# Kernel tuning notes

Hardware: AMD Instinct MI355X
Metric: run time of the kernel (lower is better)

## Reference

```python
import jax, jax.numpy as jnp
import numpy as np

V, D, DI, S, B, NI = 32000, 1024, 768, 512, 8, 197
EPS = 1e-5

def _ln(x, g, b):
    m = jnp.mean(x, axis=-1, keepdims=True)
    v = jnp.var(x, axis=-1, keepdims=True)
    return (x - m) * jax.lax.rsqrt(v + EPS) * g + b

def _pos_enc(seq_len, d):
    pos = np.arange(seq_len)[:, None].astype(np.float32)
    i = np.arange(0, d, 2).astype(np.float32)
    ang = pos / np.power(10000.0, i / d)
    pe = np.zeros((seq_len, d), dtype=np.float32)
    pe[:, 0::2] = np.sin(ang)
    pe[:, 1::2] = np.cos(ang)
    return jnp.asarray(pe)

def setup_inputs() -> dict:
    key = jax.random.key(0)
    ks = jax.random.split(key, 24)
    def rn(k, shape, scale=0.02):
        return jax.random.normal(k, shape, dtype=jnp.float32) * scale
    return {
        'tokens': jax.random.randint(ks[0], (B, S), 0, V),
        'img_emb': jax.random.normal(ks[1], (B, NI, DI), dtype=jnp.float32),
        'emb_table': rn(ks[2], (V, D), 1.0),
        'Wq1': rn(ks[3], (D, D)), 'bq1': jnp.zeros((D,), jnp.float32),
        'Wk1': rn(ks[4], (D, D)), 'bk1': jnp.zeros((D,), jnp.float32),
        'Wv1': rn(ks[5], (D, D)), 'bv1': jnp.zeros((D,), jnp.float32),
        'g1': jnp.ones((D,), jnp.float32), 'b1': jnp.zeros((D,), jnp.float32),
        'Wq2': rn(ks[6], (D, D)), 'bq2': jnp.zeros((D,), jnp.float32),
        'Wk2': rn(ks[7], (DI, D)), 'bk2': jnp.zeros((D,), jnp.float32),
        'Wv2': rn(ks[8], (DI, D)), 'bv2': jnp.zeros((D,), jnp.float32),
        'g2': jnp.ones((D,), jnp.float32), 'b2': jnp.zeros((D,), jnp.float32),
        'Wp': rn(ks[9], (D, V)), 'bp': jnp.zeros((V,), jnp.float32),
    }

def _forward(tokens, img_emb, emb_table, Wq1, bq1, Wk1, bk1, Wv1, bv1, g1, b1,
             Wq2, bq2, Wk2, bk2, Wv2, bv2, g2, b2, Wp, bp):
    scale = 1.0 / jnp.sqrt(jnp.float32(D))
    x = emb_table[tokens] + _pos_enc(S, D)[None]  # [B,S,D]
    # masked (causal) self-attention
    Q = x @ Wq1 + bq1
    K = x @ Wk1 + bk1
    Vv = x @ Wv1 + bv1
    attn = jnp.einsum('bqd,bkd->bqk', Q, K) * scale
    causal = jnp.tril(jnp.ones((S, S), dtype=bool))
    attn = jnp.where(causal[None], attn, -jnp.inf)
    A = jax.nn.softmax(attn, axis=-1)
    x = _ln(A @ Vv + x, g1, b1)
    # cross-attention over image tokens
    Q2 = x @ Wq2 + bq2
    K2 = img_emb @ Wk2 + bk2
    V2 = img_emb @ Wv2 + bv2
    A2 = jax.nn.softmax(jnp.einsum('bqd,bkd->bqk', Q2, K2) * scale, axis=-1)
    x = _ln(A2 @ V2 + x, g2, b2)
    # vocab projection (note: Decoder.forward never calls self.ff)
    return x @ Wp + bp  # [B,S,V]

def reference(tokens, img_emb, emb_table, Wq1, bq1, Wk1, bk1, Wv1, bv1, g1, b1,
              Wq2, bq2, Wk2, bk2, Wv2, bv2, g2, b2, Wp, bp):
    return _forward(tokens, img_emb, emb_table, Wq1, bq1, Wk1, bk1, Wv1, bv1, g1, b1,
                    Wq2, bq2, Wk2, bk2, Wv2, bv2, g2, b2, Wp, bp)
```

## Files before the change

### kernel.cpp

```cpp
#include <hip/hip_runtime.h>
#include <hip/hip_bf16.h>


#define DEV __device__ __forceinline__

typedef __bf16 bf16x8 __attribute__((ext_vector_type(8)));
typedef float f32x4 __attribute__((ext_vector_type(4)));
typedef float f32x16 __attribute__((ext_vector_type(16)));
typedef unsigned int u32;
typedef __hip_bfloat16 bf16;

DEV void llds16(const void* g, void* l) {
  __builtin_amdgcn_global_load_lds((const __attribute__((address_space(1))) u32*)g,
                                   (__attribute__((address_space(3))) u32*)l, 16, 0, 0);
}

DEV float wredsum(float v){
#pragma unroll
  for (int o = 32; o; o >>= 1) v += __shfl_xor(v, o, 64);
  return v;
}
DEV float wredmax(float v){
#pragma unroll
  for (int o = 32; o; o >>= 1) v = fmaxf(v, __shfl_xor(v, o, 64));
  return v;
}

DEV void store_out(float* p, float v){ *p = v; }
DEV void store_out(bf16* p, float v){ *p = __float2bfloat16(v); }

__global__ __launch_bounds__(512, 1) void gemm256_kernel(
    const bf16* __restrict__ A, const bf16* __restrict__ Bt, float* __restrict__ C,
    const float* __restrict__ bias, int M, int N, int K, int lda, int ldb, int ldc)
{
  __shared__ alignas(16) char lds[131072];
  const int tid  = threadIdx.x;
  const int wave = tid >> 6, lane = tid & 63;
  const int l31 = lane & 31, lh = lane >> 5;
  const int wr = wave >> 2, wc = wave & 3;
  const int koff = (((lane & 3) ^ ((lane >> 3) & 3)) << 3);

  const int nbx = M >> 8;
  const int nwg = nbx * (N >> 8);
  int id = blockIdx.x;
  int g = (nwg & 7) ? id : ((id & 7) * (nwg >> 3) + (id >> 3));
  const int row0 = (g % nbx) * 256, col0 = (g / nbx) * 256;
  const int NT = K >> 5;
  const int srow = lane >> 2;

  auto stageA = [&](int t) {
    char* base = lds + (t & 3) * 32768;
    const int kk = (t << 5) + koff;
#pragma unroll
    for (int j = 0; j < 2; j++) {
      const int seg = j * 8 + wave;
      llds16(A + (long)(row0 + seg * 16 + srow) * lda + kk, base + seg * 1024);
    }
  };
  auto stageB = [&](int t) {
    char* base = lds + (t & 3) * 32768 + 16384;
    const int kk = (t << 5) + koff;
#pragma unroll
    for (int j = 0; j < 2; j++) {
      const int seg = j * 8 + wave;
      llds16(Bt + (long)(col0 + seg * 16 + srow) * ldb + kk, base + seg * 1024);
    }
  };

  f32x16 acc[4][2] = {};

  stageA(0); stageB(0); stageA(1); stageB(1); stageA(2); stageB(2);
  asm volatile("s_waitcnt vmcnt(8)" ::: "memory");
  __builtin_amdgcn_s_barrier();
  __builtin_amdgcn_sched_barrier(0);

  for (int t = 0; t < NT; t++) {
    const char* As = lds + (t & 3) * 32768;
    const char* Bs = As + 16384;
    bf16x8 af[4][2], bfv[2][2];
#pragma unroll
    for (int m = 0; m < 4; m++) {
      const int r = wr * 128 + m * 32 + l31;
      const int key = (r >> 1) & 3;
#pragma unroll
      for (int ks = 0; ks < 2; ks++)
        af[m][ks] = *(const bf16x8*)(As + (r << 6) + (((lh + 2 * ks) ^ key) << 4));
    }
#pragma unroll
    for (int n = 0; n < 2; n++) {
      const int r = wc * 64 + n * 32 + l31;
      const int key = (r >> 1) & 3;
#pragma unroll
      for (int ks = 0; ks < 2; ks++)
        bfv[n][ks] = *(const bf16x8*)(Bs + (r << 6) + (((lh + 2 * ks) ^ key) << 4));
    }
    if (t + 3 < NT) { stageA(t + 3); stageB(t + 3); }
    __builtin_amdgcn_sched_barrier(0);
    __builtin_amdgcn_s_setprio(1);
#pragma unroll
    for (int m = 0; m < 4; m++)
#pragma unroll
      for (int n = 0; n < 2; n++)
#pragma unroll
        for (int ks = 0; ks < 2; ks++)
          acc[m][n] = __builtin_amdgcn_mfma_f32_32x32x16_bf16(af[m][ks], bfv[n][ks], acc[m][n], 0, 0, 0);
    __builtin_amdgcn_s_setprio(0);
    __builtin_amdgcn_sched_barrier(0);
    if (t < NT - 3)       asm volatile("s_waitcnt vmcnt(8)" ::: "memory");
    else if (t == NT - 3) asm volatile("s_waitcnt vmcnt(4)" ::: "memory");
    else                  asm volatile("s_waitcnt vmcnt(0)" ::: "memory");
    __builtin_amdgcn_s_barrier();
    __builtin_amdgcn_sched_barrier(0);
  }

#pragma unroll
  for (int n = 0; n < 2; n++) {
    const int c = col0 + wc * 64 + n * 32 + l31;
    const float bb = bias ? bias[c] : 0.0f;
#pragma unroll
    for (int m = 0; m < 4; m++) {
      const int rb = row0 + wr * 128 + m * 32 + 4 * lh;
#pragma unroll
      for (int r = 0; r < 16; r++) {
        const int row = rb + (r & 3) + 8 * (r >> 2);
        C[(long)row * ldc + c] = acc[m][n][r] + bb;
      }
    }
  }
}

template<typename OutT>
__global__ __launch_bounds__(256) void gemm_bt_kernel(
    const bf16* __restrict__ A, const bf16* __restrict__ Bt, OutT* __restrict__ C,
    const float* __restrict__ bias, int M, int N, int K,
    int lda, int ldb, int ldc, long sA, long sB, long sC)
{
  A  += (long)blockIdx.z * sA;
  Bt += (long)blockIdx.z * sB;
  C  += (long)blockIdx.z * sC;
  __shared__ alignas(16) bf16 As[128*32];
  __shared__ alignas(16) bf16 Bs[128*32];
  const int tid = threadIdx.x;
  const int wave = tid >> 6, lane = tid & 63;
  const int lo = lane & 15, hi = lane >> 4;
  const int hi2 = hi ^ ((lo >> 1) & 3);
  const int wr = wave >> 1, wc = wave & 1;
  const int row0 = blockIdx.x * 128, col0 = blockIdx.y * 128;
  const int srow  = lane >> 2;
  const int skoff = (((lane & 3) ^ ((lane >> 3) & 3)) << 3);

  f32x4 acc[4][4] = {};

  for (int k0 = 0; k0 < K; k0 += 32) {
#pragma unroll
    for (int c = 0; c < 2; ++c) {
      const int seg = c*4 + wave;
      int ra = row0 + seg*16 + srow; ra = ra < M ? ra : M-1;
      llds16(A + (long)ra*lda + (k0 + skoff), (char*)As + seg*1024);
      int rb = col0 + seg*16 + srow; rb = rb < N ? rb : N-1;
      llds16(Bt + (long)rb*ldb + (k0 + skoff), (char*)Bs + seg*1024);
    }
    __syncthreads();
    bf16x8 af[4], bfv[4];
#pragma unroll
    for (int m = 0; m < 4; m++)
      af[m] = *(const bf16x8*)((const char*)As + (wr*64 + m*16 + lo)*64 + hi2*16);
#pragma unroll
    for (int n = 0; n < 4; n++)
      bfv[n] = *(const bf16x8*)((const char*)Bs + (wc*64 + n*16 + lo)*64 + hi2*16);
#pragma unroll
    for (int m = 0; m < 4; m++)
#pragma unroll
      for (int n = 0; n < 4; n++)
        acc[m][n] = __builtin_amdgcn_mfma_f32_16x16x32_bf16(af[m], bfv[n], acc[m][n], 0, 0, 0);
    __syncthreads();
  }

#pragma unroll
  for (int m = 0; m < 4; m++) {
    const int rbase = row0 + wr*64 + m*16 + hi*4;
#pragma unroll
    for (int n = 0; n < 4; n++) {
      const int cc = col0 + wc*64 + n*16 + lo;
      if (cc >= N) continue;
      const float bb = bias ? bias[cc] : 0.0f;
#pragma unroll
      for (int j = 0; j < 4; j++) {
        const int rr = rbase + j;
        if (rr < M) store_out(&C[(long)rr*ldc + cc], acc[m][n][j] + bb);
      }
    }
  }
}

__global__ __launch_bounds__(256) void wprep4_kernel(
    const float* W0, const float* W1, const float* W2, const float* W3,
    bf16* T0, bf16* T1, bf16* T2, bf16* T3, int K, int N)
{
  const int z = blockIdx.z;
  const float* W = z == 0 ? W0 : z == 1 ? W1 : z == 2 ? W2 : W3;
  bf16* T = z == 0 ? T0 : z == 1 ? T1 : z == 2 ? T2 : T3;
  __shared__ bf16 t[32][33];
  const int k0 = blockIdx.x * 32, n0 = blockIdx.y * 32;
  const int tx = threadIdx.x & 31, ty = threadIdx.x >> 5;
#pragma unroll
  for (int i = 0; i < 4; i++)
    t[ty + i*8][tx] = __float2bfloat16(W[(long)(k0 + ty + i*8)*N + n0 + tx]);
  __syncthreads();
#pragma unroll
  for (int i = 0; i < 4; i++)
    T[(long)(n0 + ty + i*8)*K + k0 + tx] = t[tx][ty + i*8];
}

__global__ __launch_bounds__(256) void transpose_pad_kernel(
    const bf16* __restrict__ in, bf16* __restrict__ out,
    int R, int Cc, int inLD, int outLD, long inBatch, long outBatch)
{
  in  += (long)blockIdx.z * inBatch;
  out += (long)blockIdx.z * outBatch;
  __shared__ bf16 t[32][33];
  const int r0 = blockIdx.x * 32, c0 = blockIdx.y * 32;
  const int tx = threadIdx.x & 31, ty = threadIdx.x >> 5;
#pragma unroll
  for (int i = 0; i < 4; i++) {
    const int r = r0 + ty + i*8;
    bf16 v = __float2bfloat16(0.0f);
    if (r < R) v = in[(long)r*inLD + c0 + tx];
    t[ty + i*8][tx] = v;
  }
  __syncthreads();
#pragma unroll
  for (int i = 0; i < 4; i++) {
    const int oc = r0 + tx;
    const int orow = c0 + ty + i*8;
    if (oc < outLD) out[(long)orow*outLD + oc] = t[tx][ty + i*8];
  }
}

__global__ __launch_bounds__(256) void concat_bias_kernel(
    const float* a, const float* b, const float* c, int n1, int n2, int n3, float* out)
{
  const int i = blockIdx.x * 256 + threadIdx.x;
  if (i >= n1 + n2 + n3) return;
  out[i] = i < n1 ? a[i] : (i < n1 + n2 ? b[i - n1] : c[i - n1 - n2]);
}

__global__ __launch_bounds__(256) void embed_kernel(
    const int* __restrict__ tok, const float* __restrict__ tbl,
    float* __restrict__ xf, bf16* __restrict__ xb)
{
  const int row = blockIdx.x;
  const int s = row & 511;
  const float pos = (float)s;
  const float* te = tbl + (long)tok[row] * 1024;
  const int d0 = threadIdx.x * 4;
  float4 v = *(const float4*)(te + d0);
  float o[4] = {v.x, v.y, v.z, v.w};
#pragma unroll
  for (int k = 0; k < 4; k++) {
    const int d = d0 + k;
    const int i2 = d & ~1;
    const float ang = pos * powf(10000.0f, -(float)i2 * (1.0f/1024.0f));
    o[k] += (d & 1) ? cosf(ang) : sinf(ang);
  }
  *(float4*)(xf + (long)row*1024 + d0) = make_float4(o[0], o[1], o[2], o[3]);
#pragma unroll
  for (int k = 0; k < 4; k++) xb[(long)row*1024 + d0 + k] = __float2bfloat16(o[k]);
}

__global__ __launch_bounds__(256) void cvt_bf16_kernel(const float* __restrict__ in, bf16* __restrict__ out, long n)
{
  long i = (long)blockIdx.x * blockDim.x + threadIdx.x;
  if (i < n) out[i] = __float2bfloat16(in[i]);
}

__global__ __launch_bounds__(64) void softmax_causal_kernel(
    const float* __restrict__ Sc, bf16* __restrict__ P)
{
  const int row = blockIdx.x;
  const int q = row & 511;
  const float* srow = Sc + (long)row * 512;
  bf16* prow = P + (long)row * 512;
  const int lane = threadIdx.x;
  const float scale = 0.03125f;
  float mx = -1e30f;
  for (int j = lane; j <= q; j += 64) mx = fmaxf(mx, srow[j]);
  mx = wredmax(mx);
  float sum = 0.0f;
  for (int j = lane; j <= q; j += 64) sum += expf((srow[j] - mx) * scale);
  sum = wredsum(sum);
  const float inv = 1.0f / sum;
  for (int j = lane; j < 512; j += 64) {
    float p = (j <= q) ? expf((srow[j] - mx) * scale) * inv : 0.0f;
    prow[j] = __float2bfloat16(p);
  }
}

__global__ __launch_bounds__(64) void softmax_cross_kernel(
    const float* __restrict__ Sc, bf16* __restrict__ P)
{
  const int row = blockIdx.x;
  const float* srow = Sc + (long)row * 224;
  bf16* prow = P + (long)row * 224;
  const int lane = threadIdx.x;
  const float scale = 0.03125f;
  float mx = -1e30f;
  for (int j = lane; j < 197; j += 64) mx = fmaxf(mx, srow[j]);
  mx = wredmax(mx);
  float sum = 0.0f;
  for (int j = lane; j < 197; j += 64) sum += expf((srow[j] - mx) * scale);
  sum = wredsum(sum);
  const float inv = 1.0f / sum;
  for (int j = lane; j < 224; j += 64) {
    float p = (j < 197) ? expf((srow[j] - mx) * scale) * inv : 0.0f;
    prow[j] = __float2bfloat16(p);
  }
}

__global__ __launch_bounds__(256) void add_ln_kernel(
    const float* __restrict__ Acc, const float* __restrict__ Res,
    const float* __restrict__ g, const float* __restrict__ b,
    float* __restrict__ outf, bf16* __restrict__ outb)
{
  const int row = blockIdx.x;
  const float* a = Acc + (long)row * 1024;
  const float* r = Res + (long)row * 1024;
  float vals[4], s = 0.0f, ss = 0.0f;
#pragma unroll
  for (int i = 0; i < 4; i++) {
    const int d = threadIdx.x + i*256;
    const float v = a[d] + r[d];
    vals[i] = v; s += v; ss += v*v;
  }
  s = wredsum(s); ss = wredsum(ss);
  __shared__ float sh[8];
  const int wave = threadIdx.x >> 6, lane = threadIdx.x & 63;
  if (lane == 0) { sh[wave] = s; sh[wave+4] = ss; }
  __syncthreads();
  s  = sh[0] + sh[1] + sh[2] + sh[3];
  ss = sh[4] + sh[5] + sh[6] + sh[7];
  const float mean = s * (1.0f/1024.0f);
  const float var  = ss * (1.0f/1024.0f) - mean*mean;
  const float inv  = rsqrtf(var + 1e-5f);
#pragma unroll
  for (int i = 0; i < 4; i++) {
    const int d = threadIdx.x + i*256;
    const float y = (vals[i] - mean) * inv * g[d] + b[d];
    if (outf) outf[(long)row*1024 + d] = y;
    outb[(long)row*1024 + d] = __float2bfloat16(y);
  }
}

extern "C" void kernel_launch(void* const* d_in, const int* in_sizes, int n_in,
                              void* d_out, int out_size, void* d_ws, size_t ws_size,
                              hipStream_t stream) {
  const int*   tokens = (const int*)  d_in[0];
  const float* img    = (const float*)d_in[1];
  const float* emb    = (const float*)d_in[2];
  const float* Wq1    = (const float*)d_in[3];
  const float* bq1    = (const float*)d_in[4];
  const float* Wk1    = (const float*)d_in[5];
  const float* bk1    = (const float*)d_in[6];
  const float* Wv1    = (const float*)d_in[7];
  const float* bv1    = (const float*)d_in[8];
  const float* g1     = (const float*)d_in[9];
  const float* b1     = (const float*)d_in[10];
  const float* Wq2    = (const float*)d_in[11];
  const float* bq2    = (const float*)d_in[12];
  const float* Wk2    = (const float*)d_in[13];
  const float* bk2    = (const float*)d_in[14];
  const float* Wv2    = (const float*)d_in[15];
  const float* bv2    = (const float*)d_in[16];
  const float* g2     = (const float*)d_in[17];
  const float* b2     = (const float*)d_in[18];
  const float* Wp     = (const float*)d_in[19];
  const float* bp     = (const float*)d_in[20];
  float* out = (float*)d_out;

  const int B = 8, S = 512, D = 1024, DI = 768, NI = 197, NIP = 224, V = 32000;
  const int M = B * S;
  const int MI = B * NI;

  char* ws = (char*)d_ws;
  size_t off = 0;
  auto alloc = [&](size_t bytes) -> char* {
    char* p = ws + off; off += (bytes + 255) & ~(size_t)255; return p;
  };
  bf16* Wq1t = (bf16*)alloc((size_t)D*D*2);
  bf16* Wk1t = (bf16*)alloc((size_t)D*D*2);
  bf16* Wv1t = (bf16*)alloc((size_t)D*D*2);
  bf16* Wq2t = (bf16*)alloc((size_t)D*D*2);
  bf16* Wk2t = (bf16*)alloc((size_t)D*DI*2);
  bf16* Wv2t = (bf16*)alloc((size_t)D*DI*2);
  bf16* Wpt  = (bf16*)alloc((size_t)V*D*2);
  float* bqkv= (float*)alloc((size_t)3*D*4);
  float* bkv2= (float*)alloc((size_t)2*D*4);
  float* xf  = (float*)alloc((size_t)M*D*4);
  bf16*  xb  = (bf16*) alloc((size_t)M*D*2);
  bf16*  imgb= (bf16*) alloc((size_t)MI*DI*2);
  bf16*  QKV = (bf16*) alloc((size_t)M*3*D*2);
  bf16*  Vt  = (bf16*) alloc((size_t)M*D*2);
  float* sc1 = (float*)alloc((size_t)B*S*S*4);
  bf16*  P1  = (bf16*) alloc((size_t)B*S*S*2);
  float* ao1 = (float*)alloc((size_t)M*D*4);
  float* x2f = (float*)alloc((size_t)M*D*4);
  bf16*  x2b = (bf16*) alloc((size_t)M*D*2);
  bf16*  Q2  = (bf16*) alloc((size_t)M*D*2);
  bf16*  KV2 = (bf16*) alloc((size_t)MI*2*D*2);
  bf16*  V2t = (bf16*) alloc((size_t)B*D*NIP*2);
  float* sc2 = (float*)alloc((size_t)B*S*NIP*4);
  bf16*  P2  = (bf16*) alloc((size_t)B*S*NIP*2);
  float* ao2 = (float*)alloc((size_t)M*D*4);
  bf16*  x3b = (bf16*) alloc((size_t)M*D*2);
  (void)ws_size; (void)in_sizes; (void)n_in; (void)out_size;

  wprep4_kernel<<<dim3(D/32,  D/32, 4), 256, 0, stream>>>(Wq1, Wk1, Wv1, Wq2, Wq1t, Wk1t, Wv1t, Wq2t, D, D);
  wprep4_kernel<<<dim3(DI/32, D/32, 2), 256, 0, stream>>>(Wk2, Wv2, nullptr, nullptr, Wk2t, Wv2t, nullptr, nullptr, DI, D);
  wprep4_kernel<<<dim3(D/32,  V/32, 1), 256, 0, stream>>>(Wp, nullptr, nullptr, nullptr, Wpt, nullptr, nullptr, nullptr, D, V);
  concat_bias_kernel<<<(3*D+255)/256, 256, 0, stream>>>(bq1, bk1, bv1, D, D, D, bqkv);
  concat_bias_kernel<<<(2*D+255)/256, 256, 0, stream>>>(bk2, bv2, nullptr, D, D, 0, bkv2);

  embed_kernel<<<M, 256, 0, stream>>>(tokens, emb, xf, xb);
  {
    long n = (long)MI * DI;
    cvt_bf16_kernel<<<(int)((n + 255)/256), 256, 0, stream>>>(img, imgb, n);
  }

  auto gemmF = [&](const bf16* A, const bf16* Bt, float* C, const float* bias,
                   int m, int n, int k, int lda, int ldb, int ldc,
                   long sA, long sB, long sC, int batch) {
    dim3 g((m+127)/128, (n+127)/128, batch);
    gemm_bt_kernel<float><<<g, 256, 0, stream>>>(A, Bt, C, bias, m, n, k, lda, ldb, ldc, sA, sB, sC);
  };
  auto gemmB = [&](const bf16* A, const bf16* Bt, bf16* C, const float* bias,
                   int m, int n, int k, int lda, int ldb, int ldc,
                   long sA, long sB, long sC, int batch) {
    dim3 g((m+127)/128, (n+127)/128, batch);
    gemm_bt_kernel<bf16><<<g, 256, 0, stream>>>(A, Bt, C, bias, m, n, k, lda, ldb, ldc, sA, sB, sC);
  };

  gemmB(xb, Wq1t, QKV, bqkv, M, 3*D, D, D, D, 3*D, 0, 0, 0, 1);
  transpose_pad_kernel<<<dim3(S/32, D/32, B), 256, 0, stream>>>(
      QKV + 2*D, Vt, S, D, 3*D, S, (long)S*3*D, (long)D*S);
  gemmF(QKV, QKV + D, sc1, nullptr, S, S, D, 3*D, 3*D, S, (long)S*3*D, (long)S*3*D, (long)S*S, B);
  softmax_causal_kernel<<<M, 64, 0, stream>>>(sc1, P1);
  gemmF(P1, Vt, ao1, nullptr, S, D, S, S, S, D, (long)S*S, (long)D*S, (long)S*D, B);
  add_ln_kernel<<<M, 256, 0, stream>>>(ao1, xf, g1, b1, x2f, x2b);

  gemmB(x2b, Wq2t, Q2, bq2, M, D, D, D, D, D, 0, 0, 0, 1);
  gemmB(imgb, Wk2t, KV2, bkv2, MI, 2*D, DI, DI, DI, 2*D, 0, 0, 0, 1);
  transpose_pad_kernel<<<dim3((NIP+31)/32, D/32, B), 256, 0, stream>>>(
      KV2 + D, V2t, NI, D, 2*D, NIP, (long)NI*2*D, (long)D*NIP);
  gemmF(Q2, KV2, sc2, nullptr, S, NI, D, D, 2*D, NIP, (long)S*D, (long)NI*2*D, (long)S*NIP, B);
  softmax_cross_kernel<<<M, 64, 0, stream>>>(sc2, P2);
  gemmF(P2, V2t, ao2, nullptr, S, D, NIP, NIP, NIP, D, (long)S*NIP, (long)D*NIP, (long)S*D, B);
  add_ln_kernel<<<M, 256, 0, stream>>>(ao2, x2f, g2, b2, nullptr, x3b);

  {
    dim3 g((M/256) * (V/256));
    gemm256_kernel<<<g, 512, 0, stream>>>(x3b, Wpt, out, bp, M, V, D, D, D, V);
  }
}
```

Before: 722.7 us.

## Switch big GEMM to 16x16x32 MFMA with double-buffered LDS pipeline

Reworks the 256x256 vocab-projection GEMM kernel. The 4-stage LDS ring with 3-deep prefetch becomes a 2-stage double buffer (LDS halved). The 32x32x16 MFMA tiles become 16x16x32 MFMAs with new fragment indexing and swizzle, and the epilogue is rewritten to match. Launch bounds are raised to allow more blocks per CU. Prefetch depth drops to one tile with a full vmcnt(0) wait each iteration, which may expose more global-load latency in exchange for possible extra occupancy.

```diff
diff --git a/kernel.cpp b/kernel.cpp
--- a/kernel.cpp
+++ b/kernel.cpp
@@ -6,7 +6,6 @@
 
 typedef __bf16 bf16x8 __attribute__((ext_vector_type(8)));
 typedef float f32x4 __attribute__((ext_vector_type(4)));
-typedef float f32x16 __attribute__((ext_vector_type(16)));
 typedef unsigned int u32;
 typedef __hip_bfloat16 bf16;
 
@@ -29,14 +28,15 @@
 DEV void store_out(float* p, float v){ *p = v; }
 DEV void store_out(bf16* p, float v){ *p = __float2bfloat16(v); }
 
-__global__ __launch_bounds__(512, 1) void gemm256_kernel(
+__global__ __launch_bounds__(512, 4) void gemm256_kernel(
     const bf16* __restrict__ A, const bf16* __restrict__ Bt, float* __restrict__ C,
     const float* __restrict__ bias, int M, int N, int K, int lda, int ldb, int ldc)
 {
-  __shared__ alignas(16) char lds[131072];
+  __shared__ alignas(16) char lds[65536];
   const int tid  = threadIdx.x;
   const int wave = tid >> 6, lane = tid & 63;
-  const int l31 = lane & 31, lh = lane >> 5;
+  const int lo = lane & 15, hi = lane >> 4;
+  const int hi2 = hi ^ ((lo >> 1) & 3);
   const int wr = wave >> 2, wc = wave & 3;
   const int koff = (((lane & 3) ^ ((lane >> 3) & 3)) << 3);
 
@@ -49,7 +49,7 @@
   const int srow = lane >> 2;
 
   auto stageA = [&](int t) {
-    char* base = lds + (t & 3) * 32768;
+    char* base = lds + (t & 1) * 32768;
     const int kk = (t << 5) + koff;
 #pragma unroll
     for (int j = 0; j < 2; j++) {
@@ -58,7 +58,7 @@
     }
   };
   auto stageB = [&](int t) {
-    char* base = lds + (t & 3) * 32768 + 16384;
+    char* base = lds + (t & 1) * 32768 + 16384;
     const int kk = (t << 5) + koff;
 #pragma unroll
     for (int j = 0; j < 2; j++) {
@@ -67,64 +67,58 @@
     }
   };
 
-  f32x16 acc[4][2] = {};
-
-  stageA(0); stageB(0); stageA(1); stageB(1); stageA(2); stageB(2);
-  asm volatile("s_waitcnt vmcnt(8)" ::: "memory");
+  f32x4 acc[8][4] = {};
+
+  stageA(0); stageB(0);
+  asm volatile("s_waitcnt vmcnt(0)" ::: "memory");
   __builtin_amdgcn_s_barrier();
   __builtin_amdgcn_sched_barrier(0);
 
   for (int t = 0; t < NT; t++) {
-    const char* As = lds + (t & 3) * 32768;
+    const char* As = lds + (t & 1) * 32768;
     const char* Bs = As + 16384;
-    bf16x8 af[4][2], bfv[2][2];
-#pragma unroll
-    for (int m = 0; m < 4; m++) {
-      const int r = wr * 128 + m * 32 + l31;
-      const int key = (r >> 1) & 3;
-#pragma unroll
-      for (int ks = 0; ks < 2; ks++)
-        af[m][ks] = *(const bf16x8*)(As + (r << 6) + (((lh + 2 * ks) ^ key) << 4));
-    }
-#pragma unroll
-    for (int n = 0; n < 2; n++) {
-      const int r = wc * 64 + n * 32 + l31;
-      const int key = (r >> 1) & 3;
-#pragma unroll
-      for (int ks = 0; ks < 2; ks++)
-        bfv[n][ks] = *(const bf16x8*)(Bs + (r << 6) + (((lh + 2 * ks) ^ key) << 4));
-    }
-    if (t + 3 < NT) { stageA(t + 3); stageB(t + 3); }
-    __builtin_amdgcn_sched_barrier(0);
+    if (t + 1 < NT) { stageA(t + 1); stageB(t + 1); }
+    bf16x8 af[4], bfv[4];
+#pragma unroll
+    for (int n = 0; n < 4; n++)
+      bfv[n] = *(const bf16x8*)(Bs + ((wc * 64 + n * 16 + lo) << 6) + (hi2 << 4));
+#pragma unroll
+    for (int m = 0; m < 4; m++)
+      af[m] = *(const bf16x8*)(As + ((wr * 128 + m * 16 + lo) << 6) + (hi2 << 4));
     __builtin_amdgcn_s_setprio(1);
 #pragma unroll
     for (int m = 0; m < 4; m++)
 #pragma unroll
-      for (int n = 0; n < 2; n++)
-#pragma unroll
-        for (int ks = 0; ks < 2; ks++)
-          acc[m][n] = __builtin_amdgcn_mfma_f32_32x32x16_bf16(af[m][ks], bfv[n][ks], acc[m][n], 0, 0, 0);
+      for (int n = 0; n < 4; n++)
+        acc[m][n] = __builtin_amdgcn_mfma_f32_16x16x32_bf16(af[m], bfv[n], acc[m][n], 0, 0, 0);
+    __builtin_amdgcn_s_setprio(0);
+#pragma unroll
+    for (int m = 0; m < 4; m++)
+      af[m] = *(const bf16x8*)(As + ((wr * 128 + (m + 4) * 16 + lo) << 6) + (hi2 << 4));
+    __builtin_amdgcn_s_setprio(1);
+#pragma unroll
+    for (int m = 0; m < 4; m++)
+#pragma unroll
+      for (int n = 0; n < 4; n++)
+        acc[m + 4][n] = __builtin_amdgcn_mfma_f32_16x16x32_bf16(af[m], bfv[n], acc[m + 4][n], 0, 0, 0);
     __builtin_amdgcn_s_setprio(0);
     __builtin_amdgcn_sched_barrier(0);
-    if (t < NT - 3)       asm volatile("s_waitcnt vmcnt(8)" ::: "memory");
-    else if (t == NT - 3) asm volatile("s_waitcnt vmcnt(4)" ::: "memory");
-    else                  asm volatile("s_waitcnt vmcnt(0)" ::: "memory");
+    asm volatile("s_waitcnt vmcnt(0)" ::: "memory");
+    __builtin_amdgcn_sched_barrier(0);
     __builtin_amdgcn_s_barrier();
     __builtin_amdgcn_sched_barrier(0);
   }
 
 #pragma unroll
-  for (int n = 0; n < 2; n++) {
-    const int c = col0 + wc * 64 + n * 32 + l31;
-    const float bb = bias ? bias[c] : 0.0f;
-#pragma unroll
-    for (int m = 0; m < 4; m++) {
-      const int rb = row0 + wr * 128 + m * 32 + 4 * lh;
-#pragma unroll
-      for (int r = 0; r < 16; r++) {
-        const int row = rb + (r & 3) + 8 * (r >> 2);
-        C[(long)row * ldc + c] = acc[m][n][r] + bb;
-      }
+  for (int m = 0; m < 8; m++) {
+    const int r = row0 + wr * 128 + m * 16 + hi * 4;
+#pragma unroll
+    for (int n = 0; n < 4; n++) {
+      const int c = col0 + wc * 64 + n * 16 + lo;
+      const float bb = bias ? bias[c] : 0.0f;
+#pragma unroll
+      for (int j = 0; j < 4; j++)
+        C[(long)(r + j) * ldc + c] = acc[m][n][j] + bb;
     }
   }
 }
```

Result: slower. 2.688 ms (+271.9%).
